# Optimization experiments

Measured on AMD Instinct MI355X. Metric: run time of the kernel, lower is better.

## Reference

```python
import jax, jax.numpy as jnp
import numpy as np

DIM = 1024          # d_model
DI = 2 * DIM        # d_inner (expand=2)
DSTATE = 16         # SSM state size
DCONV = 4           # causal conv width
DTRANK = DIM // 16  # dt_rank = ceil(dim/16) = 64
B_, L = 2, 2048


def setup_inputs() -> dict:
    key = jax.random.key(0)
    ks = jax.random.split(key, 8)
    s = lambda k, shape, sc=0.02: jax.random.normal(k, shape, jnp.float32) * sc
    return {
        "x": jax.random.normal(ks[0], (B_, L, DIM), jnp.float32),
        "ln_w": jnp.ones((DIM,), jnp.float32),
        "ln_b": jnp.zeros((DIM,), jnp.float32),
        "in_proj_w": s(ks[1], (2 * DI, DIM)),
        "conv_w": s(ks[2], (DI, 1, DCONV), 0.1),
        "conv_b": jnp.zeros((DI,), jnp.float32),
        "x_proj_w": s(ks[3], (DTRANK + 2 * DSTATE, DI)),
        "dt_proj_w": s(ks[4], (DI, DTRANK), 0.1),
        # standard Mamba dt bias init: softplus^{-1}(0.01)
        "dt_proj_b": jnp.log(jnp.expm1(jnp.full((DI,), 0.01, jnp.float32))),
        # S4D-real init: A = -[1..d_state]
        "A_log": jnp.log(jnp.broadcast_to(jnp.arange(1, DSTATE + 1, dtype=jnp.float32), (DI, DSTATE))),
        "D": jnp.ones((DI,), jnp.float32),
        "out_proj_w": s(ks[5], (DIM, DI)),
    }


def _layernorm(x, w, b, eps=1e-5):
    mu = x.mean(-1, keepdims=True)
    var = ((x - mu) ** 2).mean(-1, keepdims=True)
    return (x - mu) * jax.lax.rsqrt(var + eps) * w + b


def _silu(x):
    return x * jax.nn.sigmoid(x)


def _mamba(x, in_proj_w, conv_w, conv_b, x_proj_w, dt_proj_w, dt_proj_b, A_log, D, out_proj_w):
    b, l, _ = x.shape
    xz = x @ in_proj_w.T                      # [b,l,2*DI]
    xc, z = jnp.split(xz, 2, axis=-1)
    # depthwise causal conv over time
    xt = jnp.pad(xc.transpose(0, 2, 1), ((0, 0), (0, 0), (DCONV - 1, 0)))
    xt = jax.lax.conv_general_dilated(
        xt, conv_w, (1,), 'VALID',
        dimension_numbers=('NCH', 'OIH', 'NCH'), feature_group_count=DI)
    xc = _silu(xt + conv_b[None, :, None]).transpose(0, 2, 1)  # [b,l,DI]
    # input-dependent dt, B, C
    dbc = xc @ x_proj_w.T
    dt = dbc[..., :DTRANK]
    Bm = dbc[..., DTRANK:DTRANK + DSTATE]     # [b,l,n]
    Cm = dbc[..., DTRANK + DSTATE:]           # [b,l,n]
    delta = jax.nn.softplus(dt @ dt_proj_w.T + dt_proj_b)  # [b,l,DI]
    A = -jnp.exp(A_log)                        # [DI,n]
    dA = jnp.exp(delta[..., None] * A)         # [b,l,DI,n]
    dBu = (delta * xc)[..., None] * Bm[:, :, None, :]  # [b,l,DI,n]

    def step(h, inp):
        dA_t, dBu_t, C_t = inp
        h = dA_t * h + dBu_t                   # [b,DI,n]
        return h, jnp.einsum('bdn,bn->bd', h, C_t)

    h0 = jnp.zeros((b, DI, DSTATE), x.dtype)
    _, ys = jax.lax.scan(step, h0,
                         (dA.transpose(1, 0, 2, 3), dBu.transpose(1, 0, 2, 3), Cm.transpose(1, 0, 2)))
    y = ys.transpose(1, 0, 2) + xc * D         # [b,l,DI]
    y = y * _silu(z)
    return y @ out_proj_w.T


def reference(x, ln_w, ln_b, in_proj_w, conv_w, conv_b, x_proj_w, dt_proj_w, dt_proj_b, A_log, D, out_proj_w):
    # single block: x = x + Mamba(LN(x))
    return x + _mamba(_layernorm(x, ln_w, ln_b), in_proj_w, conv_w, conv_b,
                      x_proj_w, dt_proj_w, dt_proj_b, A_log, D, out_proj_w)
```

## Files before the change

### kernel.cpp

```cpp
#include <hip/hip_runtime.h>
#include <hip/hip_bf16.h>
#include <math.h>

#define DIM 1024
#define DI 2048
#define DSTATE 16
#define DTRANK 64
#define NB 2
#define L_ 2048
#define M_TOT (NB*L_)
#define NCHUNK 64
#define CLEN (L_/NCHUNK)

typedef unsigned short u16;
typedef float f32x4 __attribute__((ext_vector_type(4)));
typedef __bf16 bf16x8 __attribute__((ext_vector_type(8)));

static __device__ __forceinline__ float bf2f(u16 u){
  union{float f;unsigned int i;}x; x.i = ((unsigned int)u)<<16; return x.f;
}
static __device__ __forceinline__ u16 f2bf(float f){
  union{float f;unsigned int u;}v; v.f=f;
  unsigned int x = v.u;
  return (u16)((x + 0x7fffu + ((x>>16)&1u)) >> 16);
}
static __device__ __forceinline__ void gload16(const void* g, void* l){
  __builtin_amdgcn_global_load_lds(
      (const __attribute__((address_space(1))) unsigned int*)g,
      (__attribute__((address_space(3))) unsigned int*)l, 16, 0, 0);
}

#define N4_WIN  1048576
#define N4_WDT  32768
#define N4_WOUT 524288
#define NB_CAST3 ((N4_WIN+N4_WDT+N4_WOUT)/256)
#define NB_XPROJ 256
#define NB_LN    M_TOT
__global__ __launch_bounds__(256) void fused_pre_k(
    const float* __restrict__ in_proj_w, const float* __restrict__ dt_proj_w,
    const float* __restrict__ out_proj_w, const float* __restrict__ x_proj_w,
    const float* __restrict__ x, const float* __restrict__ lw, const float* __restrict__ lb,
    u16* __restrict__ win, u16* __restrict__ wdt, u16* __restrict__ wout,
    u16* __restrict__ wxp, u16* __restrict__ xn){
  const int bid = blockIdx.x, t = threadIdx.x;
  if (bid < NB_CAST3){
    int i = bid*256 + t;
    const float* s; u16* o; int j;
    if (i < N4_WIN){ s = in_proj_w; o = win; j = i; }
    else if (i < N4_WIN+N4_WDT){ s = dt_proj_w; o = wdt; j = i - N4_WIN; }
    else { s = out_proj_w; o = wout; j = i - N4_WIN - N4_WDT; }
    float4 v = reinterpret_cast<const float4*>(s)[j];
    ushort4 ov; ov.x=f2bf(v.x); ov.y=f2bf(v.y); ov.z=f2bf(v.z); ov.w=f2bf(v.w);
    reinterpret_cast<ushort4*>(o)[j] = ov;
    return;
  }
  if (bid < NB_CAST3 + NB_XPROJ){
    int i = (bid - NB_CAST3)*256 + t;
    int row = (i*4) >> 11;
    ushort4 o;
    if (row < 96){
      float4 v = reinterpret_cast<const float4*>(x_proj_w)[i];
      o.x=f2bf(v.x); o.y=f2bf(v.y); o.z=f2bf(v.z); o.w=f2bf(v.w);
    } else { o.x=0;o.y=0;o.z=0;o.w=0; }
    reinterpret_cast<ushort4*>(wxp)[i] = o;
    return;
  }
  const int row = bid - NB_CAST3 - NB_XPROJ;
  const float4 v = reinterpret_cast<const float4*>(x + (size_t)row*DIM)[t];
  float s = v.x+v.y+v.z+v.w;
  float q = v.x*v.x+v.y*v.y+v.z*v.z+v.w*v.w;
  #pragma unroll
  for (int o=1;o<64;o<<=1){ s += __shfl_xor(s,o); q += __shfl_xor(q,o); }
  __shared__ float ss[4], sq[4];
  if ((t&63)==0){ ss[t>>6]=s; sq[t>>6]=q; }
  __syncthreads();
  s = ss[0]+ss[1]+ss[2]+ss[3]; q = sq[0]+sq[1]+sq[2]+sq[3];
  const float mu = s*(1.f/DIM);
  const float rs = rsqrtf(q*(1.f/DIM) - mu*mu + 1e-5f);
  const float4 wv = reinterpret_cast<const float4*>(lw)[t];
  const float4 bv = reinterpret_cast<const float4*>(lb)[t];
  ushort4 o;
  o.x = f2bf((v.x-mu)*rs*wv.x + bv.x);
  o.y = f2bf((v.y-mu)*rs*wv.y + bv.y);
  o.z = f2bf((v.z-mu)*rs*wv.z + bv.z);
  o.w = f2bf((v.w-mu)*rs*wv.w + bv.w);
  reinterpret_cast<ushort4*>(xn + (size_t)row*DIM)[t] = o;
}

template<int MODE, int NSPLIT>
__global__ __launch_bounds__(512,1) void ring256(
    const u16* __restrict__ A, const u16* __restrict__ Bw, int K, int nbn, int nblk,
    u16* __restrict__ b0, u16* __restrict__ b1){
  constexpr int TILE = 256*32;
  constexpr int BUFE = 2*TILE;
  __shared__ u16 lds[4*BUFE];
  const int t = threadIdx.x;
  const int w = t>>6, lane = t&63;
  const int wr = w>>2, wc = w&3;
  const int nwg = gridDim.x;
  int wg = blockIdx.x;
  wg = (wg&7)*(nwg>>3) + (wg>>3);
  const int ks  = (NSPLIT>1)? wg/nblk : 0;
  const int rem = (NSPLIT>1)? wg%nblk : wg;
  const int SN = nbn>>2;
  const int s4 = rem>>4, j4 = rem&15;
  const int bm = (s4/SN)*4 + (j4>>2);
  const int bn = (s4%SN)*4 + (j4&3);
  const int row0 = bm*256, col0 = bn*256;
  const int Kpart = K/NSPLIT, kbase = ks*Kpart, nt = Kpart>>5;

  const int r0 = t>>2;
  const int cc = (t&3) ^ ((r0>>1)&3);
  const u16* gA0 = A + (size_t)(row0 + r0)*K + kbase + cc*8;
  const u16* gA1 = gA0 + (size_t)128*K;
  const u16* gB0 = Bw + (size_t)(col0 + r0)*K + kbase + cc*8;
  const u16* gB1 = gB0 + (size_t)128*K;
  const int baseA0 = (w<<10), baseA1 = (w<<10)+8192;
  const int baseB0 = 16384+(w<<10), baseB1 = 16384+8192+(w<<10);

  f32x4 acc[8][4];
  #pragma unroll
  for (int m=0;m<8;m++)
    #pragma unroll
    for (int n=0;n<4;n++) acc[m][n] = (f32x4){0.f,0.f,0.f,0.f};

  int offA[8], offB[4];
  #pragma unroll
  for (int m=0;m<8;m++){
    const int ra = wr*128 + m*16 + (lane&15);
    offA[m] = ra*32 + (((lane>>4) ^ ((ra>>1)&3))<<3);
  }
  #pragma unroll
  for (int n=0;n<4;n++){
    const int rb = wc*64 + n*16 + (lane&15);
    offB[n] = TILE + rb*32 + (((lane>>4) ^ ((rb>>1)&3))<<3);
  }

  for (int p=0;p<3 && p<nt;++p){
    char* bp = (char*)lds + (size_t)p*(BUFE*2);
    gload16(gA0, bp+baseA0); gload16(gA1, bp+baseA1);
    gload16(gB0, bp+baseB0); gload16(gB1, bp+baseB1);
    gA0 += 32; gA1 += 32; gB0 += 32; gB1 += 32;
  }

  for (int t2=0;t2<nt;++t2){
    const int left = nt-1-t2;
    if (left>=2)      asm volatile("s_waitcnt vmcnt(8)" ::: "memory");
    else if (left==1) asm volatile("s_waitcnt vmcnt(4)" ::: "memory");
    else              asm volatile("s_waitcnt vmcnt(0)" ::: "memory");
    __builtin_amdgcn_s_barrier();
    if (t2+3<nt){
      char* bp = (char*)lds + (size_t)((t2+3)&3)*(BUFE*2);
      gload16(gA0, bp+baseA0); gload16(gA1, bp+baseA1);
      gload16(gB0, bp+baseB0); gload16(gB1, bp+baseB1);
      gA0 += 32; gA1 += 32; gB0 += 32; gB1 += 32;
    }
    const u16* Lb = lds + (size_t)(t2&3)*BUFE;
    bf16x8 af[8], bfv[4];
    #pragma unroll
    for (int m=0;m<8;m++) af[m] = *reinterpret_cast<const bf16x8*>(&Lb[offA[m]]);
    #pragma unroll
    for (int n=0;n<4;n++) bfv[n] = *reinterpret_cast<const bf16x8*>(&Lb[offB[n]]);
    __builtin_amdgcn_s_setprio(1);
    #pragma unroll
    for (int m=0;m<8;m++)
      #pragma unroll
      for (int n=0;n<4;n++)
        acc[m][n] = __builtin_amdgcn_mfma_f32_16x16x32_bf16(af[m], bfv[n], acc[m][n], 0,0,0);
    __builtin_amdgcn_s_setprio(0);
  }

  const int rb4 = (lane>>4)*4, lc = lane&15;
  #pragma unroll
  for (int m=0;m<8;m++){
    #pragma unroll
    for (int n=0;n<4;n++){
      #pragma unroll
      for (int i=0;i<4;i++){
        const int row = row0 + wr*128 + m*16 + rb4 + i;
        const int col = col0 + wc*64 + n*16 + lc;
        const float v = acc[m][n][i];
        if (MODE==1){
          if (col < DI) b0[(size_t)row*DI + col] = f2bf(v);
          else          b1[(size_t)row*DI + col - DI] = f2bf(v);
        } else {
          b0[((size_t)ks*M_TOT + row)*1024 + col] = f2bf(v);
        }
      }
    }
  }
}

template<int MODE, int NSPLIT>
__global__ __launch_bounds__(256,2) void ring_gemm(
    const u16* __restrict__ A, const u16* __restrict__ Bw, int K, int nbn, int nblk,
    float* __restrict__ f0, u16* __restrict__ b0,
    const float* __restrict__ e0){
  constexpr int BM = 128;
  constexpr int TILE_ELEMS = BM*32;
  constexpr int BUF_BYTES = TILE_ELEMS*2*2;
  __shared__ u16 lds0[4*2*TILE_ELEMS];
  const int t = threadIdx.x;
  const int w = t >> 6, lane = t & 63;
  const int lrow = lane & 15;
  const int nwg = gridDim.x;
  int wg = blockIdx.x;
  wg = (wg & 7)*(nwg >> 3) + (wg >> 3);
  const int ks  = (NSPLIT > 1) ? (wg / nblk) : 0;
  const int rem = (NSPLIT > 1) ? (wg % nblk) : wg;
  const int bm = rem / nbn, bn = rem % nbn;
  const int row0 = bm*BM, col0 = bn*BM;
  const int wr = (w>>1)*64, wc = (w&1)*64;
  const int Kpart = K / NSPLIT;
  const int kbase = ks * Kpart;
  const int nt = Kpart >> 5;

  const int srow = t >> 2;
  const int schunk = ((t&3) ^ ((t>>3)&3))*8;
  const u16* gA0 = A + (size_t)(row0 + srow)*K + kbase + schunk;
  const u16* gA1 = gA0 + (size_t)64*K;
  const u16* gB0 = Bw + (size_t)(col0 + srow)*K + kbase + schunk;
  const u16* gB1 = gB0 + (size_t)64*K;
  const int baseA0 = (w*16)*64;
  const int baseA1 = (64 + w*16)*64;
  const int baseB0 = BM*64 + baseA0;
  const int baseB1 = BM*64 + baseA1;

  f32x4 acc[4][4];
  #pragma unroll
  for (int m=0;m<4;m++)
    #pragma unroll
    for (int n=0;n<4;n++) acc[m][n] = (f32x4){0.f,0.f,0.f,0.f};

  const int rchunk = ((lane>>4) ^ ((lane>>1)&3))*8;

  for (int p = 0; p < 3 && p < nt; ++p){
    char* bp = (char*)lds0 + p*BUF_BYTES;
    gload16(gA0, bp + baseA0); gload16(gA1, bp + baseA1);
    gload16(gB0, bp + baseB0); gload16(gB1, bp + baseB1);
    gA0 += 32; gA1 += 32; gB0 += 32; gB1 += 32;
  }

  for (int t2 = 0; t2 < nt; ++t2){
    const int left = nt - 1 - t2;
    if (left >= 2)      asm volatile("s_waitcnt vmcnt(8)" ::: "memory");
    else if (left == 1) asm volatile("s_waitcnt vmcnt(4)" ::: "memory");
    else                asm volatile("s_waitcnt vmcnt(0)" ::: "memory");
    __builtin_amdgcn_s_barrier();
    if (t2 + 3 < nt){
      char* bp = (char*)lds0 + ((t2+3)&3)*BUF_BYTES;
      gload16(gA0, bp + baseA0); gload16(gA1, bp + baseA1);
      gload16(gB0, bp + baseB0); gload16(gB1, bp + baseB1);
      gA0 += 32; gA1 += 32; gB0 += 32; gB1 += 32;
    }
    const u16* Lb = (const u16*)((const char*)lds0 + (t2&3)*BUF_BYTES);
    bf16x8 af[4], bfv[4];
    #pragma unroll
    for (int m=0;m<4;m++)
      af[m] = *reinterpret_cast<const bf16x8*>(&Lb[(wr + m*16 + lrow)*32 + rchunk]);
    #pragma unroll
    for (int n=0;n<4;n++)
      bfv[n] = *reinterpret_cast<const bf16x8*>(&Lb[TILE_ELEMS + (wc + n*16 + lrow)*32 + rchunk]);
    __builtin_amdgcn_s_setprio(1);
    #pragma unroll
    for (int m=0;m<4;m++)
      #pragma unroll
      for (int n=0;n<4;n++)
        acc[m][n] = __builtin_amdgcn_mfma_f32_16x16x32_bf16(af[m], bfv[n], acc[m][n], 0,0,0);
    __builtin_amdgcn_s_setprio(0);
  }

  const int rb = (lane>>4)*4;
  #pragma unroll
  for (int m=0;m<4;m++){
    #pragma unroll
    for (int n=0;n<4;n++){
      #pragma unroll
      for (int i=0;i<4;i++){
        const int row = row0 + wr + m*16 + rb + i;
        const int col = col0 + wc + n*16 + lrow;
        const float v = acc[m][n][i];
        if (MODE==3){
          const float xv = v + e0[col];
          const float sp = (xv > 20.f) ? xv : log1pf(__expf(xv));
          b0[(size_t)row*DI + col] = f2bf(sp);
        } else {
          f0[((size_t)ks*M_TOT + row)*128 + col] = v;
        }
      }
    }
  }
}

__global__ __launch_bounds__(256) void reduce_xp_k(const float* __restrict__ P,
    float* __restrict__ dbc, u16* __restrict__ dtb){
  const int tid = blockIdx.x*256 + threadIdx.x;
  const int m = tid >> 5, c4 = tid & 31;
  f32x4 s = (f32x4){0.f,0.f,0.f,0.f};
  #pragma unroll
  for (int k=0;k<8;k++)
    s += *reinterpret_cast<const f32x4*>(&P[((size_t)k*M_TOT + m)*128 + c4*4]);
  *reinterpret_cast<f32x4*>(&dbc[(size_t)m*128 + c4*4]) = s;
  if (c4 < 16){
    ushort4 o; o.x=f2bf(s.x); o.y=f2bf(s.y); o.z=f2bf(s.z); o.w=f2bf(s.w);
    *reinterpret_cast<ushort4*>(&dtb[(size_t)m*DTRANK + c4*4]) = o;
  }
}

__global__ __launch_bounds__(256) void reduce_out_k(const u16* __restrict__ P,
    const float* __restrict__ x, float* __restrict__ out){
  const size_t i = ((size_t)blockIdx.x*256 + threadIdx.x)*4;
  f32x4 r = *reinterpret_cast<const f32x4*>(&x[i]);
  #pragma unroll
  for (int k=0;k<4;k++){
    ushort4 a = *reinterpret_cast<const ushort4*>(&P[(size_t)k*M_TOT*1024 + i]);
    r.x += bf2f(a.x); r.y += bf2f(a.y); r.z += bf2f(a.z); r.w += bf2f(a.w);
  }
  *reinterpret_cast<f32x4*>(&out[i]) = r;
}

__global__ __launch_bounds__(256) void conv_silu_k(const u16* __restrict__ xc,
    const float* __restrict__ cw, const float* __restrict__ cb, u16* __restrict__ out){
  const int idx = blockIdx.x*256 + threadIdx.x;
  const int m = idx >> 9;
  const int dq = idx & 511;
  const int d0 = dq*4;
  const int l = m & (L_-1);
  float wgt[4][4];
  #pragma unroll
  for (int j=0;j<4;j++){
    float4 t4 = reinterpret_cast<const float4*>(cw)[d0+j];
    wgt[j][0]=t4.x; wgt[j][1]=t4.y; wgt[j][2]=t4.z; wgt[j][3]=t4.w;
  }
  const float4 bb = reinterpret_cast<const float4*>(cb)[dq];
  float acc[4] = {bb.x, bb.y, bb.z, bb.w};
  #pragma unroll
  for (int k=0;k<4;k++){
    const int ls = l + k - 3;
    if (ls >= 0){
      ushort4 xv = *reinterpret_cast<const ushort4*>(&xc[(size_t)(m+k-3)*DI + d0]);
      float xf[4] = {bf2f(xv.x), bf2f(xv.y), bf2f(xv.z), bf2f(xv.w)};
      #pragma unroll
      for (int j=0;j<4;j++) acc[j] += xf[j]*wgt[j][k];
    }
  }
  ushort4 o;
  u16 ov[4];
  #pragma unroll
  for (int j=0;j<4;j++){
    const float v = acc[j];
    ov[j] = f2bf(v / (1.f + __expf(-v)));
  }
  o.x=ov[0]; o.y=ov[1]; o.z=ov[2]; o.w=ov[3];
  *reinterpret_cast<ushort4*>(&out[(size_t)m*DI + d0]) = o;
}

__global__ __launch_bounds__(256) void scan1_k(const u16* __restrict__ delta,
    const u16* __restrict__ xc, const float* __restrict__ dbc,
    const float* __restrict__ A_log, float* __restrict__ aps, float* __restrict__ hend){
  const int bid = blockIdx.x;
  const int dblk = bid & 7;
  const int bc = bid >> 3;
  const int b = bc >> 6, c = bc & (NCHUNK-1);
  const int t = threadIdx.x;
  const int d = dblk*256 + t;
  __shared__ float Bsh[CLEN*DSTATE];
  const int mbase = b*L_ + c*CLEN;
  Bsh[t]     = dbc[(size_t)(mbase + (t>>4))*128 + 64 + (t&15)];
  Bsh[t+256] = dbc[(size_t)(mbase + 16 + (t>>4))*128 + 64 + (t&15)];
  float un[DSTATE], h[DSTATE];
  #pragma unroll
  for (int n=0;n<DSTATE;n++){
    un[n] = -__expf(A_log[d*DSTATE + n]);
    h[n] = 0.f;
  }
  __syncthreads();
  const u16* dp = delta + (size_t)mbase*DI + d;
  const u16* xp = xc    + (size_t)mbase*DI + d;
  float sdv = 0.f;
  u16 dr = dp[0];
  u16 xr = xp[0];
  for (int j=0;j<CLEN;j++){
    const int jn = (j+1 < CLEN) ? j+1 : j;
    const u16 dr_n = dp[(size_t)jn*DI];
    const u16 xr_n = xp[(size_t)jn*DI];
    const float dv = bf2f(dr);
    const float xf = bf2f(xr);
    sdv += dv;
    const float c0 = dv * xf;
    #pragma unroll
    for (int n=0;n<DSTATE;n++){
      const float dA = __expf(un[n]*dv);
      h[n] = fmaf(dA, h[n], c0 * Bsh[j*DSTATE+n]);
    }
    dr = dr_n; xr = xr_n;
  }
  float* ap_out = aps  + (size_t)bc*(DSTATE*DI) + d;
  float* he_out = hend + (size_t)bc*(DSTATE*DI) + d;
  #pragma unroll
  for (int n=0;n<DSTATE;n++){
    ap_out[(size_t)n*DI] = __expf(un[n]*sdv);
    he_out[(size_t)n*DI] = h[n];
  }
}

__global__ void combine_k(const float* __restrict__ aps, const float* __restrict__ hend,
                          float* __restrict__ hinit){
  const int gid = blockIdx.x*256 + threadIdx.x;
  const int b = gid >> 15;
  const int dn = gid & 32767;
  float h = 0.f;
  #pragma unroll 4
  for (int c=0;c<NCHUNK;c++){
    const size_t idx = (size_t)(b*NCHUNK + c)*(DI*DSTATE) + dn;
    hinit[idx] = h;
    h = hend[idx] + aps[idx]*h;
  }
}

__global__ __launch_bounds__(256) void scan2_k(const u16* __restrict__ delta,
    const u16* __restrict__ xc, const float* __restrict__ dbc,
    const u16* __restrict__ z, const float* __restrict__ A_log, const float* __restrict__ Dvec,
    const float* __restrict__ hinit, u16* __restrict__ y){
  const int bid = blockIdx.x;
  const int dblk = bid & 7;
  const int bc = bid >> 3;
  const int b = bc >> 6, c = bc & (NCHUNK-1);
  const int t = threadIdx.x;
  const int d = dblk*256 + t;
  __shared__ float Bsh[CLEN*DSTATE], Csh[CLEN*DSTATE];
  const int mbase = b*L_ + c*CLEN;
  Bsh[t]     = dbc[(size_t)(mbase + (t>>4))*128 + 64 + (t&15)];
  Bsh[t+256] = dbc[(size_t)(mbase + 16 + (t>>4))*128 + 64 + (t&15)];
  Csh[t]     = dbc[(size_t)(mbase + (t>>4))*128 + 80 + (t&15)];
  Csh[t+256] = dbc[(size_t)(mbase + 16 + (t>>4))*128 + 80 + (t&15)];
  float un[DSTATE], h[DSTATE];
  const float* hi = hinit + (size_t)bc*(DSTATE*DI) + d;
  #pragma unroll
  for (int n=0;n<DSTATE;n++){
    un[n] = -__expf(A_log[d*DSTATE+n]);
    h[n] = hi[(size_t)n*DI];
  }
  const float Dd = Dvec[d];
  __syncthreads();
  const u16* dp = delta + (size_t)mbase*DI + d;
  const u16* xp = xc    + (size_t)mbase*DI + d;
  const u16* zp = z     + (size_t)mbase*DI + d;
  u16* yp = y + (size_t)mbase*DI + d;
  u16 dr = dp[0];
  u16 xr = xp[0], zr = zp[0];
  for (int j=0;j<CLEN;j++){
    const int jn = (j+1 < CLEN) ? j+1 : j;
    const u16 dr_n = dp[(size_t)jn*DI];
    const u16 xr_n = xp[(size_t)jn*DI];
    const u16 zr_n = zp[(size_t)jn*DI];
    const float dv = bf2f(dr);
    const float xf = bf2f(xr), zf = bf2f(zr);
    const float c0 = dv * xf;
    float s = 0.f;
    #pragma unroll
    for (int n=0;n<DSTATE;n++){
      const float dA = __expf(un[n]*dv);
      h[n] = fmaf(dA, h[n], c0 * Bsh[j*DSTATE+n]);
      s = fmaf(h[n], Csh[j*DSTATE+n], s);
    }
    const float yf = fmaf(xf, Dd, s);
    const float yo = yf * (zf / (1.f + __expf(-zf)));
    yp[(size_t)j*DI] = f2bf(yo);
    dr = dr_n; xr = xr_n; zr = zr_n;
  }
}

extern "C" void kernel_launch(void* const* d_in, const int* in_sizes, int n_in,
                              void* d_out, int out_size, void* d_ws, size_t ws_size,
                              hipStream_t stream){
  const float* x         = (const float*)d_in[0];
  const float* ln_w      = (const float*)d_in[1];
  const float* ln_b      = (const float*)d_in[2];
  const float* in_proj_w = (const float*)d_in[3];
  const float* conv_w    = (const float*)d_in[4];
  const float* conv_b    = (const float*)d_in[5];
  const float* x_proj_w  = (const float*)d_in[6];
  const float* dt_proj_w = (const float*)d_in[7];
  const float* dt_proj_b = (const float*)d_in[8];
  const float* A_log     = (const float*)d_in[9];
  const float* Dvec      = (const float*)d_in[10];
  const float* out_proj_w= (const float*)d_in[11];
  float* out = (float*)d_out;

  char* w = (char*)d_ws;
  size_t off = 0;
  auto carve = [&](size_t bytes)->char*{ char* p = w + off; off += (bytes + 255) & ~(size_t)255; return p; };
  u16*   xn    = (u16*)  carve((size_t)M_TOT*DIM*2);
  u16*   win   = (u16*)  carve((size_t)2*DI*DIM*2);
  u16*   xcb   = (u16*)  carve((size_t)M_TOT*DI*2);
  u16*   zb    = (u16*)  carve((size_t)M_TOT*DI*2);
  u16*   xcv   = (u16*)  carve((size_t)M_TOT*DI*2);
  u16*   wxp   = (u16*)  carve((size_t)128*DI*2);
  u16*   dtb   = (u16*)  carve((size_t)M_TOT*DTRANK*2);
  u16*   wdt   = (u16*)  carve((size_t)DI*DTRANK*2);
  u16*   deltab= (u16*)  carve((size_t)M_TOT*DI*2);
  u16*   wout  = (u16*)  carve((size_t)DIM*DI*2);
  u16*   yb    = (u16*)  carve((size_t)M_TOT*DI*2);
  float* Pxp   = (float*)carve((size_t)8*M_TOT*128*4);
  float* dbc   = (float*)carve((size_t)M_TOT*128*4);
  float* aps   = (float*)carve((size_t)NB*NCHUNK*DI*DSTATE*4);
  float* hend  = (float*)carve((size_t)NB*NCHUNK*DI*DSTATE*4);
  float* hinit = (float*)carve((size_t)NB*NCHUNK*DI*DSTATE*4);
  u16* Pout = (u16*)aps;

  fused_pre_k<<<NB_CAST3 + NB_XPROJ + NB_LN, 256, 0, stream>>>(
      in_proj_w, dt_proj_w, out_proj_w, x_proj_w, x, ln_w, ln_b,
      win, wdt, wout, wxp, xn);

  ring256<1,1><<<256, 512, 0, stream>>>(xn, win, DIM, 16, 256, xcb, zb);

  conv_silu_k<<<(M_TOT*512)/256, 256, 0, stream>>>(xcb, conv_w, conv_b, xcv);

  ring_gemm<5,8><<<8*32, 256, 0, stream>>>(xcv, wxp, DI, 1, 32, Pxp, nullptr, nullptr);
  reduce_xp_k<<<(M_TOT*32)/256, 256, 0, stream>>>(Pxp, dbc, dtb);

  ring_gemm<3,1><<<32*16, 256, 0, stream>>>(dtb, wdt, DTRANK, 16, 512, nullptr, deltab, dt_proj_b);

  scan1_k<<<NB*NCHUNK*8, 256, 0, stream>>>(deltab, xcv, dbc, A_log, aps, hend);
  combine_k<<<(NB*DI*DSTATE)/256, 256, 0, stream>>>(aps, hend, hinit);
  scan2_k<<<NB*NCHUNK*8, 256, 0, stream>>>(deltab, xcv, dbc, zb, A_log, Dvec, hinit, yb);

  ring256<6,4><<<256, 512, 0, stream>>>(yb, wout, DI, 4, 64, Pout, nullptr);
  reduce_out_k<<<(M_TOT*1024)/(4*256), 256, 0, stream>>>(Pout, x, out);
}
```

Before: 240.4 us.

## Widen GEMM blocks to 1024 threads, reuse conv rows, pack scan state in bf16

The 256x256 GEMM kernel now runs 1024 threads (16 waves) per block, each wave holding a 64x64 sub-tile with half the accumulators and one load per operand per stage. The causal conv kernel now produces four time steps per thread from seven loaded rows, so overlapping inputs are reused. The chunked scan now writes per-chunk end state and decay as packed bf16 pairs in a single buffer instead of two fp32 buffers, halving combine traffic. This lowers the precision of the inter-chunk carry, and launch_bounds(1024,4) may be unreachable given LDS usage.

```diff
diff --git a/kernel.cpp b/kernel.cpp
--- a/kernel.cpp
+++ b/kernel.cpp
@@ -13,6 +13,7 @@
 #define CLEN (L_/NCHUNK)
 
 typedef unsigned short u16;
+typedef unsigned int u32;
 typedef float f32x4 __attribute__((ext_vector_type(4)));
 typedef __bf16 bf16x8 __attribute__((ext_vector_type(8)));
 
@@ -88,7 +89,7 @@
 }
 
 template<int MODE, int NSPLIT>
-__global__ __launch_bounds__(512,1) void ring256(
+__global__ __launch_bounds__(1024,4) void ring256(
     const u16* __restrict__ A, const u16* __restrict__ Bw, int K, int nbn, int nblk,
     u16* __restrict__ b0, u16* __restrict__ b1){
   constexpr int TILE = 256*32;
@@ -112,22 +113,20 @@
   const int r0 = t>>2;
   const int cc = (t&3) ^ ((r0>>1)&3);
   const u16* gA0 = A + (size_t)(row0 + r0)*K + kbase + cc*8;
-  const u16* gA1 = gA0 + (size_t)128*K;
   const u16* gB0 = Bw + (size_t)(col0 + r0)*K + kbase + cc*8;
-  const u16* gB1 = gB0 + (size_t)128*K;
-  const int baseA0 = (w<<10), baseA1 = (w<<10)+8192;
-  const int baseB0 = 16384+(w<<10), baseB1 = 16384+8192+(w<<10);
-
-  f32x4 acc[8][4];
-  #pragma unroll
-  for (int m=0;m<8;m++)
+  const int baseA = (w<<10);
+  const int baseB = 16384 + (w<<10);
+
+  f32x4 acc[4][4];
+  #pragma unroll
+  for (int m=0;m<4;m++)
     #pragma unroll
     for (int n=0;n<4;n++) acc[m][n] = (f32x4){0.f,0.f,0.f,0.f};
 
-  int offA[8], offB[4];
-  #pragma unroll
-  for (int m=0;m<8;m++){
-    const int ra = wr*128 + m*16 + (lane&15);
+  int offA[4], offB[4];
+  #pragma unroll
+  for (int m=0;m<4;m++){
+    const int ra = wr*64 + m*16 + (lane&15);
     offA[m] = ra*32 + (((lane>>4) ^ ((ra>>1)&3))<<3);
   }
   #pragma unroll
@@ -138,32 +137,30 @@
 
   for (int p=0;p<3 && p<nt;++p){
     char* bp = (char*)lds + (size_t)p*(BUFE*2);
-    gload16(gA0, bp+baseA0); gload16(gA1, bp+baseA1);
-    gload16(gB0, bp+baseB0); gload16(gB1, bp+baseB1);
-    gA0 += 32; gA1 += 32; gB0 += 32; gB1 += 32;
+    gload16(gA0, bp+baseA); gload16(gB0, bp+baseB);
+    gA0 += 32; gB0 += 32;
   }
 
   for (int t2=0;t2<nt;++t2){
     const int left = nt-1-t2;
-    if (left>=2)      asm volatile("s_waitcnt vmcnt(8)" ::: "memory");
-    else if (left==1) asm volatile("s_waitcnt vmcnt(4)" ::: "memory");
+    if (left>=2)      asm volatile("s_waitcnt vmcnt(4)" ::: "memory");
+    else if (left==1) asm volatile("s_waitcnt vmcnt(2)" ::: "memory");
     else              asm volatile("s_waitcnt vmcnt(0)" ::: "memory");
     __builtin_amdgcn_s_barrier();
     if (t2+3<nt){
       char* bp = (char*)lds + (size_t)((t2+3)&3)*(BUFE*2);
-      gload16(gA0, bp+baseA0); gload16(gA1, bp+baseA1);
-      gload16(gB0, bp+baseB0); gload16(gB1, bp+baseB1);
-      gA0 += 32; gA1 += 32; gB0 += 32; gB1 += 32;
+      gload16(gA0, bp+baseA); gload16(gB0, bp+baseB);
+      gA0 += 32; gB0 += 32;
     }
     const u16* Lb = lds + (size_t)(t2&3)*BUFE;
-    bf16x8 af[8], bfv[4];
-    #pragma unroll
-    for (int m=0;m<8;m++) af[m] = *reinterpret_cast<const bf16x8*>(&Lb[offA[m]]);
+    bf16x8 af[4], bfv[4];
+    #pragma unroll
+    for (int m=0;m<4;m++) af[m] = *reinterpret_cast<const bf16x8*>(&Lb[offA[m]]);
     #pragma unroll
     for (int n=0;n<4;n++) bfv[n] = *reinterpret_cast<const bf16x8*>(&Lb[offB[n]]);
     __builtin_amdgcn_s_setprio(1);
     #pragma unroll
-    for (int m=0;m<8;m++)
+    for (int m=0;m<4;m++)
       #pragma unroll
       for (int n=0;n<4;n++)
         acc[m][n] = __builtin_amdgcn_mfma_f32_16x16x32_bf16(af[m], bfv[n], acc[m][n], 0,0,0);
@@ -172,12 +169,12 @@
 
   const int rb4 = (lane>>4)*4, lc = lane&15;
   #pragma unroll
-  for (int m=0;m<8;m++){
+  for (int m=0;m<4;m++){
     #pragma unroll
     for (int n=0;n<4;n++){
       #pragma unroll
       for (int i=0;i<4;i++){
-        const int row = row0 + wr*128 + m*16 + rb4 + i;
+        const int row = row0 + wr*64 + m*16 + rb4 + i;
         const int col = col0 + wc*64 + n*16 + lc;
         const float v = acc[m][n][i];
         if (MODE==1){
@@ -322,10 +319,11 @@
 __global__ __launch_bounds__(256) void conv_silu_k(const u16* __restrict__ xc,
     const float* __restrict__ cw, const float* __restrict__ cb, u16* __restrict__ out){
   const int idx = blockIdx.x*256 + threadIdx.x;
-  const int m = idx >> 9;
+  const int mg = idx >> 9;
   const int dq = idx & 511;
   const int d0 = dq*4;
-  const int l = m & (L_-1);
+  const int m0 = mg*4;
+  const int l0 = m0 & (L_-1);
   float wgt[4][4];
   #pragma unroll
   for (int j=0;j<4;j++){
@@ -333,31 +331,38 @@
     wgt[j][0]=t4.x; wgt[j][1]=t4.y; wgt[j][2]=t4.z; wgt[j][3]=t4.w;
   }
   const float4 bb = reinterpret_cast<const float4*>(cb)[dq];
-  float acc[4] = {bb.x, bb.y, bb.z, bb.w};
-  #pragma unroll
-  for (int k=0;k<4;k++){
-    const int ls = l + k - 3;
-    if (ls >= 0){
-      ushort4 xv = *reinterpret_cast<const ushort4*>(&xc[(size_t)(m+k-3)*DI + d0]);
-      float xf[4] = {bf2f(xv.x), bf2f(xv.y), bf2f(xv.z), bf2f(xv.w)};
+  float xv[7][4];
+  #pragma unroll
+  for (int k=0;k<7;k++){
+    if (l0 + k - 3 >= 0){
+      ushort4 v = *reinterpret_cast<const ushort4*>(&xc[(size_t)(m0+k-3)*DI + d0]);
+      xv[k][0]=bf2f(v.x); xv[k][1]=bf2f(v.y); xv[k][2]=bf2f(v.z); xv[k][3]=bf2f(v.w);
+    } else {
+      xv[k][0]=0.f; xv[k][1]=0.f; xv[k][2]=0.f; xv[k][3]=0.f;
+    }
+  }
+  #pragma unroll
+  for (int jt=0;jt<4;jt++){
+    float acc[4] = {bb.x, bb.y, bb.z, bb.w};
+    #pragma unroll
+    for (int k=0;k<4;k++)
       #pragma unroll
-      for (int j=0;j<4;j++) acc[j] += xf[j]*wgt[j][k];
-    }
-  }
-  ushort4 o;
-  u16 ov[4];
-  #pragma unroll
-  for (int j=0;j<4;j++){
-    const float v = acc[j];
-    ov[j] = f2bf(v / (1.f + __expf(-v)));
-  }
-  o.x=ov[0]; o.y=ov[1]; o.z=ov[2]; o.w=ov[3];
-  *reinterpret_cast<ushort4*>(&out[(size_t)m*DI + d0]) = o;
+      for (int j=0;j<4;j++) acc[j] += xv[jt+k][j]*wgt[j][k];
+    ushort4 o;
+    u16 ov[4];
+    #pragma unroll
+    for (int j=0;j<4;j++){
+      const float v = acc[j];
+      ov[j] = f2bf(v / (1.f + __expf(-v)));
+    }
+    o.x=ov[0]; o.y=ov[1]; o.z=ov[2]; o.w=ov[3];
+    *reinterpret_cast<ushort4*>(&out[(size_t)(m0+jt)*DI + d0]) = o;
+  }
 }
 
 __global__ __launch_bounds__(256) void scan1_k(const u16* __restrict__ delta,
     const u16* __restrict__ xc, const float* __restrict__ dbc,
-    const float* __restrict__ A_log, float* __restrict__ aps, float* __restrict__ hend){
+    const float* __restrict__ A_log, u32* __restrict__ sst){
   const int bid = blockIdx.x;
   const int dblk = bid & 7;
   const int bc = bid >> 3;
@@ -395,17 +400,15 @@
     }
     dr = dr_n; xr = xr_n;
   }
-  float* ap_out = aps  + (size_t)bc*(DSTATE*DI) + d;
-  float* he_out = hend + (size_t)bc*(DSTATE*DI) + d;
+  u32* so = sst + (size_t)bc*(DSTATE*DI) + d;
   #pragma unroll
   for (int n=0;n<DSTATE;n++){
-    ap_out[(size_t)n*DI] = __expf(un[n]*sdv);
-    he_out[(size_t)n*DI] = h[n];
-  }
-}
-
-__global__ void combine_k(const float* __restrict__ aps, const float* __restrict__ hend,
-                          float* __restrict__ hinit){
+    const u32 pk = (u32)f2bf(h[n]) | ((u32)f2bf(__expf(un[n]*sdv)) << 16);
+    so[(size_t)n*DI] = pk;
+  }
+}
+
+__global__ void combine_k(const u32* __restrict__ sst, float* __restrict__ hinit){
   const int gid = blockIdx.x*256 + threadIdx.x;
   const int b = gid >> 15;
   const int dn = gid & 32767;
@@ -414,7 +417,8 @@
   for (int c=0;c<NCHUNK;c++){
     const size_t idx = (size_t)(b*NCHUNK + c)*(DI*DSTATE) + dn;
     hinit[idx] = h;
-    h = hend[idx] + aps[idx]*h;
+    const u32 pk = sst[idx];
+    h = bf2f((u16)pk) + bf2f((u16)(pk>>16))*h;
   }
 }
 
@@ -504,28 +508,27 @@
   u16*   yb    = (u16*)  carve((size_t)M_TOT*DI*2);
   float* Pxp   = (float*)carve((size_t)8*M_TOT*128*4);
   float* dbc   = (float*)carve((size_t)M_TOT*128*4);
-  float* aps   = (float*)carve((size_t)NB*NCHUNK*DI*DSTATE*4);
-  float* hend  = (float*)carve((size_t)NB*NCHUNK*DI*DSTATE*4);
+  u32*   sst   = (u32*)  carve((size_t)NB*NCHUNK*DI*DSTATE*4);
   float* hinit = (float*)carve((size_t)NB*NCHUNK*DI*DSTATE*4);
-  u16* Pout = (u16*)aps;
+  u16* Pout = (u16*)sst;
 
   fused_pre_k<<<NB_CAST3 + NB_XPROJ + NB_LN, 256, 0, stream>>>(
       in_proj_w, dt_proj_w, out_proj_w, x_proj_w, x, ln_w, ln_b,
       win, wdt, wout, wxp, xn);
 
-  ring256<1,1><<<256, 512, 0, stream>>>(xn, win, DIM, 16, 256, xcb, zb);
-
-  conv_silu_k<<<(M_TOT*512)/256, 256, 0, stream>>>(xcb, conv_w, conv_b, xcv);
+  ring256<1,1><<<256, 1024, 0, stream>>>(xn, win, DIM, 16, 256, xcb, zb);
+
+  conv_silu_k<<<(M_TOT/4*512)/256, 256, 0, stream>>>(xcb, conv_w, conv_b, xcv);
 
   ring_gemm<5,8><<<8*32, 256, 0, stream>>>(xcv, wxp, DI, 1, 32, Pxp, nullptr, nullptr);
   reduce_xp_k<<<(M_TOT*32)/256, 256, 0, stream>>>(Pxp, dbc, dtb);
 
   ring_gemm<3,1><<<32*16, 256, 0, stream>>>(dtb, wdt, DTRANK, 16, 512, nullptr, deltab, dt_proj_b);
 
-  scan1_k<<<NB*NCHUNK*8, 256, 0, stream>>>(deltab, xcv, dbc, A_log, aps, hend);
-  combine_k<<<(NB*DI*DSTATE)/256, 256, 0, stream>>>(aps, hend, hinit);
+  scan1_k<<<NB*NCHUNK*8, 256, 0, stream>>>(deltab, xcv, dbc, A_log, sst);
+  combine_k<<<(NB*DI*DSTATE)/256, 256, 0, stream>>>(sst, hinit);
   scan2_k<<<NB*NCHUNK*8, 256, 0, stream>>>(deltab, xcv, dbc, zb, A_log, Dvec, hinit, yb);
 
-  ring256<6,4><<<256, 512, 0, stream>>>(yb, wout, DI, 4, 64, Pout, nullptr);
+  ring256<6,4><<<256, 1024, 0, stream>>>(yb, wout, DI, 4, 64, Pout, nullptr);
   reduce_out_k<<<(M_TOT*1024)/(4*256), 256, 0, stream>>>(Pout, x, out);
 }
```

After: 222.9 us. 1.08x faster.
